# Optimization experiments

Hardware: AMD Instinct MI355X
Metric: run time of the kernel (lower is better)

## Reference

```python
import jax, jax.numpy as jnp
import numpy as np

K = 9            # LCN box-filter size
EPS = 1e-6


def _box_sum(x):
    """9x9 box sum with zero padding 4, separable. x: [N,H,W] -> [N,H,W]."""
    xp = x[:, None]                                  # N,1,H,W
    kh = jnp.ones((1, 1, K, 1), x.dtype)
    kw = jnp.ones((1, 1, 1, K), x.dtype)
    y = jax.lax.conv_general_dilated(xp, kh, (1, 1), [(K // 2, K // 2), (0, 0)])
    y = jax.lax.conv_general_dilated(y, kw, (1, 1), [(0, 0), (K // 2, K // 2)])
    return y[:, 0]


def _lcn(img):
    """Faithful to torch: conv weight is ones(3,3,9,9)/81, i.e. the 'mean' SUMS over
    the 3 input channels of per-pixel 9x9 box means; every output channel is identical.
    So compute channel-sum once, box-filter it, and broadcast back over channels."""
    kk = float(K * K)
    mean_local = _box_sum(img.sum(axis=1)) / kk                 # N,H,W
    mean_sq_local = _box_sum((img * img).sum(axis=1)) / kk      # N,H,W
    std_local = (mean_sq_local - mean_local * mean_local) * kk / (kk - 1.0)
    m = mean_local[:, None]                                     # N,1,H,W (broadcasts over C)
    s = std_local[:, None]
    return (img - m) / (s + EPS), m, s


def _warp(right, disp):
    """Equivalent of affine_grid(identity) + grid -= (disp*2/W, 0) + grid_sample
    (bilinear, zeros padding, align_corners=False). Since the y-coordinate is the
    identity grid, iy == row index exactly, so sampling reduces to 1-D horizontal
    bilinear interpolation at source column ix = j - disp[n,i,j]."""
    N, C, H, W = right.shape
    ix = jnp.arange(W, dtype=right.dtype)[None, None, :] - disp   # N,H,W
    x0 = jnp.floor(ix)
    wx = ix - x0                                                  # frac weight for x1
    x0i = x0.astype(jnp.int32)
    x1i = x0i + 1
    v0 = ((x0i >= 0) & (x0i < W)).astype(right.dtype)             # zeros padding masks
    v1 = ((x1i >= 0) & (x1i < W)).astype(right.dtype)
    i0 = jnp.broadcast_to(jnp.clip(x0i, 0, W - 1)[:, None], right.shape)
    i1 = jnp.broadcast_to(jnp.clip(x1i, 0, W - 1)[:, None], right.shape)
    g0 = jnp.take_along_axis(right, i0, axis=3)                   # N,C,H,W
    g1 = jnp.take_along_axis(right, i1, axis=3)
    return g0 * (v0 * (1.0 - wx))[:, None] + g1 * (v1 * wx)[:, None]


def setup_inputs() -> dict:
    key = jax.random.key(0)
    k1, k2, k3 = jax.random.split(key, 3)
    N, C, H, W = 8, 3, 720, 1280
    left_img = jax.random.uniform(k1, (N, C, H, W), dtype=jnp.float32)
    right_img = jax.random.uniform(k2, (N, C, H, W), dtype=jnp.float32)
    dispmap = jax.random.uniform(k3, (N, H, W), dtype=jnp.float32) * 64.0  # pixels
    return {"left_img": left_img, "right_img": right_img, "dispmap": dispmap}


def reference(left_img, right_img, dispmap):
    recon_img = _warp(right_img, dispmap)
    recon_img_lcn, _, _ = _lcn(recon_img)
    left_img_lcn, _, left_std_local = _lcn(left_img)
    return jnp.abs((left_img_lcn - recon_img_lcn) * left_std_local).mean()
```

## Files before the change

kernel.cpp:

```cpp
#include <hip/hip_runtime.h>

#define NB 8
#define CC 3
#define HH 720
#define WW 1280
#define EPSL 1e-6f
#define HSEG 30
#define NSEG (HH / HSEG)
#define OUTC 56
#define NSTRIP 23
#define NITER (HSEG + 8)
#define NUNIT (NSTRIP * NSEG * NB)
#define NBLK (NUNIT / 4)

__device__ __forceinline__ float bperm(int addr, float x) {
    return __int_as_float(__builtin_amdgcn_ds_bpermute(addr, __float_as_int(x)));
}

__global__ __launch_bounds__(256)
void fused_loss_kernel(const float* __restrict__ left,
                       const float* __restrict__ right,
                       const float* __restrict__ disp,
                       float* __restrict__ out)
{
    const int t    = threadIdx.x;
    const int lane = t & 63;
    const int u    = blockIdx.x * 4 + (t >> 6);
    const int strip = u % NSTRIP;
    const int hseg  = (u / NSTRIP) % NSEG;
    const int n     = u / (NSTRIP * NSEG);
    const int h0 = hseg * HSEG;
    const int gc  = strip * OUTC + lane - 4;
    const int gcc = min(max(gc, 0), WW - 1);
    const bool out_lane = (lane >= 4) && (lane < 4 + OUTC) && (gc < WW);
    const size_t plane = (size_t)HH * WW;
    const float* __restrict__ dispn  = disp  + (size_t)n * plane;
    const float* __restrict__ leftn  = left  + (size_t)n * CC * plane;
    const float* __restrict__ rightn = right + (size_t)n * CC * plane;

    const int a_m1 = ((lane + 63) & 63) << 2;
    const int a_p1 = ((lane +  1) & 63) << 2;
    const int a_m3 = ((lane + 61) & 63) << 2;
    const int a_p3 = ((lane +  3) & 63) << 2;

    float4 rg1 = make_float4(0.f,0.f,0.f,0.f);
    float4 rg2=rg1, rg3=rg1, rg4=rg1, rg5=rg1, rg6=rg1, rg7=rg1, rg8=rg1;
    float p1l0=0,p1l1=0,p1l2=0,p1r0=0,p1r1=0,p1r2=0;
    float p2l0=0,p2l1=0,p2l2=0,p2r0=0,p2r1=0,p2r2=0;
    float p3l0=0,p3l1=0,p3l2=0,p3r0=0,p3r1=0,p3r2=0;
    float p4l0=0,p4l1=0,p4l2=0,p4r0=0,p4r1=0,p4r2=0;

    const int r0 = h0 - 4;

    int rcl = min(max(r0, 0), HH - 1);
    size_t ro = (size_t)rcl * WW + gcc;
    float dA  = dispn[ro];
    float al0 = leftn[ro], al1 = leftn[plane + ro], al2 = leftn[2*plane + ro];
    rcl = min(max(r0 + 1, 0), HH - 1);
    ro  = (size_t)rcl * WW + gcc;
    float dB  = dispn[ro];
    float bl0 = leftn[ro], bl1 = leftn[plane + ro], bl2 = leftn[2*plane + ro];

    float aw0, aw1, ag00, ag01, ag10, ag11, ag20, ag21;
    {
        float ix  = (float)gc - dA;
        float x0f = floorf(ix), wx = ix - x0f;
        int x0i = (int)x0f, x1i = x0i + 1;
        float v0 = (x0i >= 0 && x0i < WW) ? 1.f : 0.f;
        float v1 = (x1i >= 0 && x1i < WW) ? 1.f : 0.f;
        int i0 = min(max(x0i, 0), WW - 1), i1 = min(max(x1i, 0), WW - 1);
        aw0 = v0 * (1.f - wx); aw1 = v1 * wx;
        size_t rb = (size_t)min(max(r0, 0), HH - 1) * WW;
        ag00 = rightn[rb + i0];           ag01 = rightn[rb + i1];
        ag10 = rightn[plane + rb + i0];   ag11 = rightn[plane + rb + i1];
        ag20 = rightn[2*plane + rb + i0]; ag21 = rightn[2*plane + rb + i1];
    }

    float4 vsum = make_float4(0.f,0.f,0.f,0.f);
    float acc = 0.f;

    for (int iter = 0; iter < NITER; ++iter) {
        const int r = r0 + iter;

        int rcl2 = min(max(r + 2, 0), HH - 1);
        size_t ro2 = (size_t)rcl2 * WW + gcc;
        float dC  = dispn[ro2];
        float cl0 = leftn[ro2], cl1 = leftn[plane + ro2], cl2 = leftn[2*plane + ro2];

        float bw0, bw1, bg00, bg01, bg10, bg11, bg20, bg21;
        {
            float ix  = (float)gc - dB;
            float x0f = floorf(ix), wx = ix - x0f;
            int x0i = (int)x0f, x1i = x0i + 1;
            float v0 = (x0i >= 0 && x0i < WW) ? 1.f : 0.f;
            float v1 = (x1i >= 0 && x1i < WW) ? 1.f : 0.f;
            int i0 = min(max(x0i, 0), WW - 1), i1 = min(max(x1i, 0), WW - 1);
            bw0 = v0 * (1.f - wx); bw1 = v1 * wx;
            size_t rb = (size_t)min(max(r + 1, 0), HH - 1) * WW;
            bg00 = rightn[rb + i0];           bg01 = rightn[rb + i1];
            bg10 = rightn[plane + rb + i0];   bg11 = rightn[plane + rb + i1];
            bg20 = rightn[2*plane + rb + i0]; bg21 = rightn[2*plane + rb + i1];
        }

        float rca = ag00*aw0 + ag01*aw1;
        float rcb = ag10*aw0 + ag11*aw1;
        float rcc = ag20*aw0 + ag21*aw1;
        bool valr = (r >= 0) && (r < HH) && (gc >= 0) && (gc < WW);
        float rx = al0 + al1 + al2;
        float ry = al0*al0 + al1*al1 + al2*al2;
        float rz = rca + rcb + rcc;
        float rw = rca*rca + rcb*rcb + rcc*rcc;
        rx = valr ? rx : 0.f;  ry = valr ? ry : 0.f;
        rz = valr ? rz : 0.f;  rw = valr ? rw : 0.f;

        float sx = bperm(a_m1, rx) + rx + bperm(a_p1, rx);
        float sy = bperm(a_m1, ry) + ry + bperm(a_p1, ry);
        float sz = bperm(a_m1, rz) + rz + bperm(a_p1, rz);
        float sw = bperm(a_m1, rw) + rw + bperm(a_p1, rw);
        float hx = bperm(a_m3, sx) + sx + bperm(a_p3, sx);
        float hy = bperm(a_m3, sy) + sy + bperm(a_p3, sy);
        float hz = bperm(a_m3, sz) + sz + bperm(a_p3, sz);
        float hw = bperm(a_m3, sw) + sw + bperm(a_p3, sw);

        vsum.x += hx; vsum.y += hy; vsum.z += hz; vsum.w += hw;

        if (iter >= 8) {
            float ml   = vsum.x * (1.f / 81.f);
            float msl  = vsum.y * (1.f / 81.f);
            float stdl = (msl - ml * ml) * (81.f / 80.f);
            float invl = __builtin_amdgcn_rcpf(stdl + EPSL);
            float mr   = vsum.z * (1.f / 81.f);
            float msr  = vsum.w * (1.f / 81.f);
            float stdr = (msr - mr * mr) * (81.f / 80.f);
            float invr = __builtin_amdgcn_rcpf(stdr + EPSL);
            if (out_lane) {
                float av, bv;
                av = (p4l0 - ml) * invl; bv = (p4r0 - mr) * invr;
                acc += fabsf((av - bv) * stdl);
                av = (p4l1 - ml) * invl; bv = (p4r1 - mr) * invr;
                acc += fabsf((av - bv) * stdl);
                av = (p4l2 - ml) * invl; bv = (p4r2 - mr) * invr;
                acc += fabsf((av - bv) * stdl);
            }
            vsum.x -= rg8.x; vsum.y -= rg8.y; vsum.z -= rg8.z; vsum.w -= rg8.w;
        }

        rg8 = rg7; rg7 = rg6; rg6 = rg5; rg5 = rg4; rg4 = rg3; rg3 = rg2; rg2 = rg1;
        rg1 = make_float4(hx, hy, hz, hw);
        p4l0=p3l0; p4l1=p3l1; p4l2=p3l2; p4r0=p3r0; p4r1=p3r1; p4r2=p3r2;
        p3l0=p2l0; p3l1=p2l1; p3l2=p2l2; p3r0=p2r0; p3r1=p2r1; p3r2=p2r2;
        p2l0=p1l0; p2l1=p1l1; p2l2=p1l2; p2r0=p1r0; p2r1=p1r1; p2r2=p1r2;
        p1l0=al0;  p1l1=al1;  p1l2=al2;  p1r0=rca;  p1r1=rcb;  p1r2=rcc;

        al0=bl0; al1=bl1; al2=bl2;
        aw0=bw0; aw1=bw1;
        ag00=bg00; ag01=bg01; ag10=bg10; ag11=bg11; ag20=bg20; ag21=bg21;
        dB=dC; bl0=cl0; bl1=cl1; bl2=cl2;
    }

#pragma unroll
    for (int off = 32; off > 0; off >>= 1)
        acc += __shfl_down(acc, off, 64);
    __shared__ float red[4];
    if (lane == 0) red[t >> 6] = acc;
    __syncthreads();
    if (t == 0) {
        float s = red[0] + red[1] + red[2] + red[3];
        const float inv_count = 1.f / ((float)NB * CC * HH * WW);
        atomicAdd(out, s * inv_count);
    }
}

extern "C" void kernel_launch(void* const* d_in, const int* in_sizes, int n_in,
                              void* d_out, int out_size, void* d_ws, size_t ws_size,
                              hipStream_t stream) {
    const float* left  = (const float*)d_in[0];
    const float* right = (const float*)d_in[1];
    const float* disp  = (const float*)d_in[2];
    float* out = (float*)d_out;

    hipMemsetAsync(out, 0, sizeof(float) * out_size, stream);

    hipLaunchKernelGGL(fused_loss_kernel, dim3(NBLK), dim3(256), 0, stream,
                       left, right, disp, out);
}
```

Before: 241.4 us.

## Move vertical box-sum ring to LDS, use 32-bit offsets, remap block tiling

The 8-deep register shift chain of float4 row sums is replaced by a shared-memory ring buffer indexed by iteration. This cuts register pressure and removes the per-iteration register moves. Global offsets now use 32-bit unsigned arithmetic with per-channel base pointers, which cheapens address computation. Blocks are remapped so that the four waves of a block cover vertically adjacent segments of the same strip, which may improve cache locality. A Newton refinement step is added to the reciprocal, and the extra LDS traffic adds per-iteration latency.

```diff
diff --git a/kernel.cpp b/kernel.cpp
--- a/kernel.cpp
+++ b/kernel.cpp
@@ -7,11 +7,11 @@
 #define EPSL 1e-6f
 #define HSEG 30
 #define NSEG (HH / HSEG)
+#define G4   (NSEG / 4)
 #define OUTC 56
 #define NSTRIP 23
 #define NITER (HSEG + 8)
-#define NUNIT (NSTRIP * NSEG * NB)
-#define NBLK (NUNIT / 4)
+#define NBLK (NB * NSTRIP * G4)
 
 __device__ __forceinline__ float bperm(int addr, float x) {
     return __int_as_float(__builtin_amdgcn_ds_bpermute(addr, __float_as_int(x)));
@@ -25,26 +25,38 @@
 {
     const int t    = threadIdx.x;
     const int lane = t & 63;
-    const int u    = blockIdx.x * 4 + (t >> 6);
-    const int strip = u % NSTRIP;
-    const int hseg  = (u / NSTRIP) % NSEG;
-    const int n     = u / (NSTRIP * NSEG);
-    const int h0 = hseg * HSEG;
+    const int wid  = t >> 6;
+
+    const int b     = blockIdx.x;
+    const int strip = b % NSTRIP;
+    const int g     = (b / NSTRIP) % G4;
+    const int n     = b / (NSTRIP * G4);
+
+    const int hseg = g * 4 + wid;
+    const int h0   = hseg * HSEG;
+
     const int gc  = strip * OUTC + lane - 4;
     const int gcc = min(max(gc, 0), WW - 1);
+    const float gcf = (float)gc;
+    const bool col_ok   = (gc >= 0) && (gc < WW);
     const bool out_lane = (lane >= 4) && (lane < 4 + OUTC) && (gc < WW);
+
     const size_t plane = (size_t)HH * WW;
-    const float* __restrict__ dispn  = disp  + (size_t)n * plane;
-    const float* __restrict__ leftn  = left  + (size_t)n * CC * plane;
-    const float* __restrict__ rightn = right + (size_t)n * CC * plane;
+    const float* __restrict__ dp  = disp  + (size_t)n * plane;
+    const float* __restrict__ lp0 = left  + (size_t)n * CC * plane;
+    const float* __restrict__ lp1 = lp0 + plane;
+    const float* __restrict__ lp2 = lp1 + plane;
+    const float* __restrict__ rp0 = right + (size_t)n * CC * plane;
+    const float* __restrict__ rp1 = rp0 + plane;
+    const float* __restrict__ rp2 = rp1 + plane;
 
     const int a_m1 = ((lane + 63) & 63) << 2;
     const int a_p1 = ((lane +  1) & 63) << 2;
     const int a_m3 = ((lane + 61) & 63) << 2;
     const int a_p3 = ((lane +  3) & 63) << 2;
 
-    float4 rg1 = make_float4(0.f,0.f,0.f,0.f);
-    float4 rg2=rg1, rg3=rg1, rg4=rg1, rg5=rg1, rg6=rg1, rg7=rg1, rg8=rg1;
+    __shared__ float4 ring[8][256];
+
     float p1l0=0,p1l1=0,p1l2=0,p1r0=0,p1r1=0,p1r2=0;
     float p2l0=0,p2l1=0,p2l2=0,p2r0=0,p2r1=0,p2r2=0;
     float p3l0=0,p3l1=0,p3l2=0,p3r0=0,p3r1=0,p3r2=0;
@@ -53,27 +65,27 @@
     const int r0 = h0 - 4;
 
     int rcl = min(max(r0, 0), HH - 1);
-    size_t ro = (size_t)rcl * WW + gcc;
-    float dA  = dispn[ro];
-    float al0 = leftn[ro], al1 = leftn[plane + ro], al2 = leftn[2*plane + ro];
+    unsigned ro = (unsigned)(rcl * WW + gcc);
+    float dA  = dp[ro];
+    float al0 = lp0[ro], al1 = lp1[ro], al2 = lp2[ro];
     rcl = min(max(r0 + 1, 0), HH - 1);
-    ro  = (size_t)rcl * WW + gcc;
-    float dB  = dispn[ro];
-    float bl0 = leftn[ro], bl1 = leftn[plane + ro], bl2 = leftn[2*plane + ro];
+    unsigned rob = (unsigned)(rcl * WW + gcc);
+    float dB  = dp[rob];
+    float bl0 = lp0[rob], bl1 = lp1[rob], bl2 = lp2[rob];
 
     float aw0, aw1, ag00, ag01, ag10, ag11, ag20, ag21;
     {
-        float ix  = (float)gc - dA;
+        float ix  = gcf - dA;
         float x0f = floorf(ix), wx = ix - x0f;
         int x0i = (int)x0f, x1i = x0i + 1;
         float v0 = (x0i >= 0 && x0i < WW) ? 1.f : 0.f;
         float v1 = (x1i >= 0 && x1i < WW) ? 1.f : 0.f;
         int i0 = min(max(x0i, 0), WW - 1), i1 = min(max(x1i, 0), WW - 1);
         aw0 = v0 * (1.f - wx); aw1 = v1 * wx;
-        size_t rb = (size_t)min(max(r0, 0), HH - 1) * WW;
-        ag00 = rightn[rb + i0];           ag01 = rightn[rb + i1];
-        ag10 = rightn[plane + rb + i0];   ag11 = rightn[plane + rb + i1];
-        ag20 = rightn[2*plane + rb + i0]; ag21 = rightn[2*plane + rb + i1];
+        unsigned rb = (unsigned)(min(max(r0, 0), HH - 1) * WW);
+        ag00 = rp0[rb + i0]; ag01 = rp0[rb + i1];
+        ag10 = rp1[rb + i0]; ag11 = rp1[rb + i1];
+        ag20 = rp2[rb + i0]; ag21 = rp2[rb + i1];
     }
 
     float4 vsum = make_float4(0.f,0.f,0.f,0.f);
@@ -82,30 +94,32 @@
     for (int iter = 0; iter < NITER; ++iter) {
         const int r = r0 + iter;
 
+        float4 old8 = ring[iter & 7][t];
+
         int rcl2 = min(max(r + 2, 0), HH - 1);
-        size_t ro2 = (size_t)rcl2 * WW + gcc;
-        float dC  = dispn[ro2];
-        float cl0 = leftn[ro2], cl1 = leftn[plane + ro2], cl2 = leftn[2*plane + ro2];
+        unsigned ro2 = (unsigned)(rcl2 * WW + gcc);
+        float dC  = dp[ro2];
+        float cl0 = lp0[ro2], cl1 = lp1[ro2], cl2 = lp2[ro2];
 
         float bw0, bw1, bg00, bg01, bg10, bg11, bg20, bg21;
         {
-            float ix  = (float)gc - dB;
+            float ix  = gcf - dB;
             float x0f = floorf(ix), wx = ix - x0f;
             int x0i = (int)x0f, x1i = x0i + 1;
             float v0 = (x0i >= 0 && x0i < WW) ? 1.f : 0.f;
             float v1 = (x1i >= 0 && x1i < WW) ? 1.f : 0.f;
             int i0 = min(max(x0i, 0), WW - 1), i1 = min(max(x1i, 0), WW - 1);
             bw0 = v0 * (1.f - wx); bw1 = v1 * wx;
-            size_t rb = (size_t)min(max(r + 1, 0), HH - 1) * WW;
-            bg00 = rightn[rb + i0];           bg01 = rightn[rb + i1];
-            bg10 = rightn[plane + rb + i0];   bg11 = rightn[plane + rb + i1];
-            bg20 = rightn[2*plane + rb + i0]; bg21 = rightn[2*plane + rb + i1];
+            unsigned rb = (unsigned)(min(max(r + 1, 0), HH - 1) * WW);
+            bg00 = rp0[rb + i0]; bg01 = rp0[rb + i1];
+            bg10 = rp1[rb + i0]; bg11 = rp1[rb + i1];
+            bg20 = rp2[rb + i0]; bg21 = rp2[rb + i1];
         }
 
         float rca = ag00*aw0 + ag01*aw1;
         float rcb = ag10*aw0 + ag11*aw1;
         float rcc = ag20*aw0 + ag21*aw1;
-        bool valr = (r >= 0) && (r < HH) && (gc >= 0) && (gc < WW);
+        bool valr = col_ok && ((unsigned)r < (unsigned)HH);
         float rx = al0 + al1 + al2;
         float ry = al0*al0 + al1*al1 + al2*al2;
         float rz = rca + rcb + rcc;
@@ -122,17 +136,23 @@
         float hz = bperm(a_m3, sz) + sz + bperm(a_p3, sz);
         float hw = bperm(a_m3, sw) + sw + bperm(a_p3, sw);
 
+        ring[iter & 7][t] = make_float4(hx, hy, hz, hw);
+
         vsum.x += hx; vsum.y += hy; vsum.z += hz; vsum.w += hw;
 
         if (iter >= 8) {
             float ml   = vsum.x * (1.f / 81.f);
             float msl  = vsum.y * (1.f / 81.f);
             float stdl = (msl - ml * ml) * (81.f / 80.f);
-            float invl = __builtin_amdgcn_rcpf(stdl + EPSL);
+            float sl   = stdl + EPSL;
+            float invl = __builtin_amdgcn_rcpf(sl);
+            invl = invl * __builtin_fmaf(-sl, invl, 2.f);
             float mr   = vsum.z * (1.f / 81.f);
             float msr  = vsum.w * (1.f / 81.f);
             float stdr = (msr - mr * mr) * (81.f / 80.f);
-            float invr = __builtin_amdgcn_rcpf(stdr + EPSL);
+            float sr   = stdr + EPSL;
+            float invr = __builtin_amdgcn_rcpf(sr);
+            invr = invr * __builtin_fmaf(-sr, invr, 2.f);
             if (out_lane) {
                 float av, bv;
                 av = (p4l0 - ml) * invl; bv = (p4r0 - mr) * invr;
@@ -142,11 +162,9 @@
                 av = (p4l2 - ml) * invl; bv = (p4r2 - mr) * invr;
                 acc += fabsf((av - bv) * stdl);
             }
-            vsum.x -= rg8.x; vsum.y -= rg8.y; vsum.z -= rg8.z; vsum.w -= rg8.w;
+            vsum.x -= old8.x; vsum.y -= old8.y; vsum.z -= old8.z; vsum.w -= old8.w;
         }
 
-        rg8 = rg7; rg7 = rg6; rg6 = rg5; rg5 = rg4; rg4 = rg3; rg3 = rg2; rg2 = rg1;
-        rg1 = make_float4(hx, hy, hz, hw);
         p4l0=p3l0; p4l1=p3l1; p4l2=p3l2; p4r0=p3r0; p4r1=p3r1; p4r2=p3r2;
         p3l0=p2l0; p3l1=p2l1; p3l2=p2l2; p3r0=p2r0; p3r1=p2r1; p3r2=p2r2;
         p2l0=p1l0; p2l1=p1l1; p2l2=p1l2; p2r0=p1r0; p2r1=p1r1; p2r2=p1r2;
@@ -161,8 +179,9 @@
 #pragma unroll
     for (int off = 32; off > 0; off >>= 1)
         acc += __shfl_down(acc, off, 64);
-    __shared__ float red[4];
-    if (lane == 0) red[t >> 6] = acc;
+    __syncthreads();
+    float* red = (float*)&ring[0][0];
+    if (lane == 0) red[wid] = acc;
     __syncthreads();
     if (t == 0) {
         float s = red[0] + red[1] + red[2] + red[3];
```

Result: no change. 244.6 us (+1.3%).
